# Performance work log

Hardware: AMD Instinct MI355X
Metric: run time of the kernel (lower is better)

The kernel has to match this reference:

```python
import jax, jax.numpy as jnp
import numpy as np

N_NODES = 100000
N_EDGES = 3200000
D_IN = 128
D_OUT = 128


def setup_inputs() -> dict:
    key = jax.random.key(0)
    k1, k2, k3 = jax.random.split(key, 3)
    x = jax.random.normal(k1, (N_NODES, D_IN), dtype=jnp.float32)
    edge_index = jax.random.randint(k2, (2, N_EDGES), 0, N_NODES, dtype=jnp.int64)
    # Glorot-style init for the GCN linear weight [out, in]
    weight = jax.random.normal(k3, (D_OUT, D_IN), dtype=jnp.float32) * (1.0 / np.sqrt(D_IN))
    bias = jnp.zeros((D_OUT,), dtype=jnp.float32)
    return {"x": x, "edge_index": edge_index, "weight": weight, "bias": bias}


def reference(x, edge_index, weight, bias):
    """LinearEncoder.forward: (GCNConv(x, edge_index), 0).

    GCNConv: out = D^-1/2 (A + I) D^-1/2 (x W^T) + b  (symmetric norm, self-loops).
    """
    n = x.shape[0]
    src = edge_index[0]
    dst = edge_index[1]
    # add self-loops
    loops = jnp.arange(n, dtype=src.dtype)
    src = jnp.concatenate([src, loops])
    dst = jnp.concatenate([dst, loops])
    # degree (in-degree over destination nodes, unit edge weights)
    ones = jnp.ones(src.shape[0], dtype=x.dtype)
    deg = jax.ops.segment_sum(ones, dst, num_segments=n)
    deg_inv_sqrt = jnp.where(deg > 0, jax.lax.rsqrt(deg), 0.0).astype(x.dtype)
    norm = deg_inv_sqrt[src] * deg_inv_sqrt[dst]  # [E+N]
    # dense transform first (as in PyG GCNConv), then sparse aggregation
    h = x @ weight.T  # [N, D_OUT]
    msgs = h[src] * norm[:, None]  # [E+N, D_OUT]
    out = jax.ops.segment_sum(msgs, dst, num_segments=n) + bias
    return (out, 0)
```

## Files before the change

### kernel.cpp

```cpp
#include <hip/hip_runtime.h>
#include <hip/hip_bf16.h>

#define N_NODES 100000
#define N_EDGES 3200000
#define D 128

typedef unsigned short u16;

#define BKT_W 512
#define NBKT 196
#define NSH 8
#define CAPS 2304
#define CAPB (NSH * CAPS)
#define EPB 6400
#define P1B 500
#define EPT 25

#define CW_BLOCKS 8

typedef __attribute__((ext_vector_type(8))) short bf16x8;
typedef __attribute__((ext_vector_type(4))) float f32x4;

__device__ __forceinline__ float bf2f(u16 u) {
    union { unsigned i; float f; } a; a.i = ((unsigned)u) << 16; return a.f;
}
__device__ __forceinline__ float asf(unsigned u) {
    union { unsigned i; float f; } a; a.i = u; return a.f;
}
__device__ __forceinline__ u16 f2bf(float f) {
    __hip_bfloat16 b = __float2bfloat16(f);
    return *(u16*)&b;
}

__global__ __launch_bounds__(256) void p1_multisplit(const int* __restrict__ ei,
                                                     int* __restrict__ bcnt,
                                                     unsigned* __restrict__ bbuf) {
    __shared__ unsigned s1[EPB];
    __shared__ unsigned s2[EPB];
    __shared__ int hist[NBKT], lbase[NBKT], cur[NBKT], gbase[NBKT];
    __shared__ int sc[256];
    int t = threadIdx.x, blk = blockIdx.x;
    int sh = blk & (NSH - 1);
    int e0 = blk * EPB;
    if (t < NBKT) hist[t] = 0;
    __syncthreads();

    unsigned char bk[EPT];
#pragma unroll
    for (int k = 0; k < EPT; ++k) {
        int i = k * 256 + t;
        int s = ei[e0 + i];
        int d = ei[N_EDGES + e0 + i];
        unsigned bkt = (unsigned)d >> 9;
        bk[k] = (unsigned char)bkt;
        s1[i] = ((unsigned)s << 9) | ((unsigned)d & 511u);
        atomicAdd(&hist[bkt], 1);
    }
    __syncthreads();

    if (t < NBKT) gbase[t] = atomicAdd(&bcnt[t * NSH + sh], hist[t]);

    sc[t] = (t < NBKT) ? hist[t] : 0;
    __syncthreads();
    for (int o = 1; o < 256; o <<= 1) {
        int u = (t >= o) ? sc[t - o] : 0;
        __syncthreads();
        sc[t] += u;
        __syncthreads();
    }
    if (t < NBKT) { int ex = sc[t] - hist[t]; lbase[t] = ex; cur[t] = ex; }
    __syncthreads();

#pragma unroll
    for (int k = 0; k < EPT; ++k) {
        int i = k * 256 + t;
        int p = atomicAdd(&cur[bk[k]], 1);
        s2[p] = s1[i];
    }
    __syncthreads();

    int wave = t >> 6, lane = t & 63;
    for (int bkt = wave; bkt < NBKT; bkt += 4) {
        int n = hist[bkt], lb = lbase[bkt], gb = gbase[bkt];
        unsigned* dst = bbuf + ((size_t)bkt * NSH + sh) * CAPS;
        for (int j = lane; j < n; j += 64) {
            int p = gb + j;
            if (p < CAPS) dst[p] = s2[lb + j];
        }
    }
}

__global__ __launch_bounds__(256) void p2_localsort(const unsigned* __restrict__ bbuf,
                                                    const int* __restrict__ bcnt,
                                                    int* __restrict__ sorted,
                                                    int* __restrict__ beg_g,
                                                    int* __restrict__ cnt_g,
                                                    float* __restrict__ dinv_g,
                                                    const float* __restrict__ w,
                                                    u16* __restrict__ wbf) {
    __shared__ int hist[BKT_W], cur[BKT_W], shcnt[NSH];
    __shared__ int sc[256];
    int b = blockIdx.x, t = threadIdx.x;

    if (b >= NBKT) {
        int idx = (b - NBKT) * 256 + t;
        const float4* wp = (const float4*)(w + (size_t)idx * 8);
        float4 a = wp[0], bb = wp[1];
        union { u16 h[8]; uint4 v; } o;
        o.h[0] = f2bf(a.x); o.h[1] = f2bf(a.y);
        o.h[2] = f2bf(a.z); o.h[3] = f2bf(a.w);
        o.h[4] = f2bf(bb.x); o.h[5] = f2bf(bb.y);
        o.h[6] = f2bf(bb.z); o.h[7] = f2bf(bb.w);
        ((uint4*)wbf)[idx] = o.v;
        return;
    }

    if (t < NSH) { int m = bcnt[b * NSH + t]; shcnt[t] = m > CAPS ? CAPS : m; }
    hist[t] = 0; hist[t + 256] = 0;
    __syncthreads();

    for (int sh = 0; sh < NSH; ++sh) {
        int m = shcnt[sh];
        const unsigned* p = bbuf + ((size_t)b * NSH + sh) * CAPS;
        for (int i = t; i < m; i += 256) atomicAdd(&hist[p[i] & 511u], 1);
    }
    __syncthreads();

    int a0 = hist[2 * t], a1 = hist[2 * t + 1];
    sc[t] = a0 + a1;
    __syncthreads();
    for (int o = 1; o < 256; o <<= 1) {
        int u = (t >= o) ? sc[t - o] : 0;
        __syncthreads();
        sc[t] += u;
        __syncthreads();
    }
    int exp_ = sc[t] - a0 - a1;
    cur[2 * t] = exp_;
    cur[2 * t + 1] = exp_ + a0;
    __syncthreads();

#pragma unroll
    for (int q = 0; q < 2; ++q) {
        int l = t + q * 256;
        int node = b * BKT_W + l;
        if (node < N_NODES) {
            int c = hist[l];
            cnt_g[node] = c;
            beg_g[node] = b * CAPB + cur[l];
            dinv_g[node] = rsqrtf((float)(c + 1));
        }
    }
    __syncthreads();

    int* dst = sorted + (size_t)b * CAPB;
    for (int sh = 0; sh < NSH; ++sh) {
        int m = shcnt[sh];
        const unsigned* p = bbuf + ((size_t)b * NSH + sh) * CAPS;
        for (int i = t; i < m; i += 256) {
            unsigned ww = p[i];
            int pp = atomicAdd(&cur[ww & 511u], 1);
            dst[pp] = (int)(ww >> 9);
        }
    }
}

__global__ __launch_bounds__(256) void gemm_h(const float* __restrict__ x,
                                              const u16* __restrict__ wbf,
                                              const float* __restrict__ dinv,
                                              u16* __restrict__ h) {
    int t = threadIdx.x;
    int wave = t >> 6, lane = t & 63;
    int n0 = blockIdx.x * 64 + wave * 16;
    int lrow = lane & 15;
    int quad = lane >> 4;

    int arow = n0 + lrow;
    const float* ap = x + (size_t)(arow < N_NODES ? arow : 0) * D;
    bf16x8 afrag[4];
#pragma unroll
    for (int kt = 0; kt < 4; ++kt) {
        int k0 = kt * 32 + quad * 8;
        f32x4 x0 = *(const f32x4*)(ap + k0);
        f32x4 x1 = *(const f32x4*)(ap + k0 + 4);
        bf16x8 a;
        a[0] = (short)f2bf(x0.x); a[1] = (short)f2bf(x0.y);
        a[2] = (short)f2bf(x0.z); a[3] = (short)f2bf(x0.w);
        a[4] = (short)f2bf(x1.x); a[5] = (short)f2bf(x1.y);
        a[6] = (short)f2bf(x1.z); a[7] = (short)f2bf(x1.w);
        afrag[kt] = a;
    }

    float dsc[4];
#pragma unroll
    for (int i = 0; i < 4; ++i) {
        int n = n0 + quad * 4 + i;
        dsc[i] = (n < N_NODES) ? dinv[n] : 0.f;
    }

#pragma unroll
    for (int jt = 0; jt < 8; ++jt) {
        int j0 = jt * 16;
        f32x4 acc = {0.f, 0.f, 0.f, 0.f};
#pragma unroll
        for (int kt = 0; kt < 4; ++kt) {
            int k0 = kt * 32 + quad * 8;
            bf16x8 b = *(const bf16x8*)(wbf + (size_t)(j0 + lrow) * D + k0);
            acc = __builtin_amdgcn_mfma_f32_16x16x32_bf16(afrag[kt], b, acc, 0, 0, 0);
        }
#pragma unroll
        for (int i = 0; i < 4; ++i) {
            int n = n0 + quad * 4 + i;
            if (n < N_NODES) h[(size_t)n * D + j0 + lrow] = f2bf(acc[i] * dsc[i]);
        }
    }
}

__global__ __launch_bounds__(256) void aggregate_h(const u16* __restrict__ h,
                                                   const float* __restrict__ dinv,
                                                   const int* __restrict__ beg_g,
                                                   const int* __restrict__ cnt_g,
                                                   const int* __restrict__ sorted_src,
                                                   const float* __restrict__ bias,
                                                   float* __restrict__ out) {
    int w = threadIdx.x >> 6;
    int l = threadIdx.x & 63;
    int n = blockIdx.x * 4 + w;
    const unsigned* h32 = (const unsigned*)h;

    unsigned us = h32[(size_t)n * 64 + l];
    float acc0 = asf(us << 16);
    float acc1 = asf(us & 0xffff0000u);

    int c = __builtin_amdgcn_readfirstlane(cnt_g[n]);
    int beg = __builtin_amdgcn_readfirstlane(beg_g[n]);
    const int* sp = sorted_src + beg;

    int i = 0;
    for (; i + 16 <= c; i += 16) {
        int s[16];
#pragma unroll
        for (int j = 0; j < 16; ++j) s[j] = sp[i + j];
        unsigned u[16];
#pragma unroll
        for (int j = 0; j < 16; ++j) u[j] = h32[(size_t)s[j] * 64 + l];
#pragma unroll
        for (int j = 0; j < 16; ++j) {
            acc0 += asf(u[j] << 16);
            acc1 += asf(u[j] & 0xffff0000u);
        }
    }
    for (; i + 4 <= c; i += 4) {
        int s0 = sp[i], s1 = sp[i + 1], s2 = sp[i + 2], s3 = sp[i + 3];
        unsigned u0 = h32[(size_t)s0 * 64 + l];
        unsigned u1 = h32[(size_t)s1 * 64 + l];
        unsigned u2 = h32[(size_t)s2 * 64 + l];
        unsigned u3 = h32[(size_t)s3 * 64 + l];
        acc0 += asf(u0 << 16); acc1 += asf(u0 & 0xffff0000u);
        acc0 += asf(u1 << 16); acc1 += asf(u1 & 0xffff0000u);
        acc0 += asf(u2 << 16); acc1 += asf(u2 & 0xffff0000u);
        acc0 += asf(u3 << 16); acc1 += asf(u3 & 0xffff0000u);
    }
    for (; i < c; ++i) {
        unsigned u = h32[(size_t)sp[i] * 64 + l];
        acc0 += asf(u << 16); acc1 += asf(u & 0xffff0000u);
    }

    float dn = dinv[n];
    float2 bs = ((const float2*)bias)[l];
    float2 o;
    o.x = acc0 * dn + bs.x;
    o.y = acc1 * dn + bs.y;
    ((float2*)out)[(size_t)n * 64 + l] = o;

    if (blockIdx.x == 0 && threadIdx.x == 0) out[(size_t)N_NODES * D] = 0.f;
}

extern "C" void kernel_launch(void* const* d_in, const int* in_sizes, int n_in,
                              void* d_out, int out_size, void* d_ws, size_t ws_size,
                              hipStream_t stream) {
    const float* x = (const float*)d_in[0];
    const int* ei = (const int*)d_in[1];
    const float* w = (const float*)d_in[2];
    const float* bias = (const float*)d_in[3];
    float* out = (float*)d_out;

    char* ws = (char*)d_ws;
    size_t o = 0;
    auto alloc = [&](size_t bytes) -> char* {
        char* p = ws + o;
        o = (o + bytes + 511) & ~(size_t)511;
        return p;
    };
    char* regionA = alloc((size_t)N_NODES * D * 2);
    unsigned* bbuf = (unsigned*)regionA;
    u16* h = (u16*)regionA;
    int* sorted = (int*)alloc((size_t)NBKT * CAPB * 4);
    int* cnt = (int*)alloc((size_t)N_NODES * 4);
    int* beg = (int*)alloc((size_t)N_NODES * 4);
    float* dinv = (float*)alloc((size_t)N_NODES * 4);
    int* bcnt = (int*)alloc((size_t)NBKT * NSH * 4);
    u16* wbf = (u16*)alloc((size_t)D * D * 2);

    hipMemsetAsync(bcnt, 0, (size_t)NBKT * NSH * 4, stream);

    p1_multisplit<<<P1B, 256, 0, stream>>>(ei, bcnt, bbuf);
    p2_localsort<<<NBKT + CW_BLOCKS, 256, 0, stream>>>(bbuf, bcnt, sorted, beg, cnt, dinv, w, wbf);
    gemm_h<<<(N_NODES + 63) / 64, 256, 0, stream>>>(x, wbf, dinv, h);
    aggregate_h<<<N_NODES / 4, 256, 0, stream>>>(h, dinv, beg, cnt, sorted, bias, out);
}
```

Measured before the change: 322.1 us.

## Replace two-pass bucket sort with global atomic counting sort, overlap scatter with GEMM

Builds the CSR by destination with a global atomic degree count, a decoupled block-prefix scan using an atomic running total, and an atomic-cursor scatter of source ids. The scatter runs in the same launch as the MFMA GEMM so the two overlap. This drops the multisplit and local-sort staging buffers and their capacity clamps. In exchange it relies on heavy global atomics. Because the scan blocks take their offsets in arbitrary order, each node's edge segment lands at a nondeterministic place, though it stays contiguous.

Result: slower. 645.6 us (+100.4%).

```diff
diff --git a/kernel.cpp b/kernel.cpp
--- a/kernel.cpp
+++ b/kernel.cpp
@@ -7,16 +7,10 @@
 
 typedef unsigned short u16;
 
-#define BKT_W 512
-#define NBKT 196
-#define NSH 8
-#define CAPS 2304
-#define CAPB (NSH * CAPS)
-#define EPB 6400
-#define P1B 500
-#define EPT 25
-
+#define S1B 3125
 #define CW_BLOCKS 8
+#define SCB 3125
+#define GEMM_B 1563
 
 typedef __attribute__((ext_vector_type(8))) short bf16x8;
 typedef __attribute__((ext_vector_type(4))) float f32x4;
@@ -32,78 +26,21 @@
     return *(u16*)&b;
 }
 
-__global__ __launch_bounds__(256) void p1_multisplit(const int* __restrict__ ei,
-                                                     int* __restrict__ bcnt,
-                                                     unsigned* __restrict__ bbuf) {
-    __shared__ unsigned s1[EPB];
-    __shared__ unsigned s2[EPB];
-    __shared__ int hist[NBKT], lbase[NBKT], cur[NBKT], gbase[NBKT];
-    __shared__ int sc[256];
-    int t = threadIdx.x, blk = blockIdx.x;
-    int sh = blk & (NSH - 1);
-    int e0 = blk * EPB;
-    if (t < NBKT) hist[t] = 0;
-    __syncthreads();
-
-    unsigned char bk[EPT];
-#pragma unroll
-    for (int k = 0; k < EPT; ++k) {
-        int i = k * 256 + t;
-        int s = ei[e0 + i];
-        int d = ei[N_EDGES + e0 + i];
-        unsigned bkt = (unsigned)d >> 9;
-        bk[k] = (unsigned char)bkt;
-        s1[i] = ((unsigned)s << 9) | ((unsigned)d & 511u);
-        atomicAdd(&hist[bkt], 1);
-    }
-    __syncthreads();
-
-    if (t < NBKT) gbase[t] = atomicAdd(&bcnt[t * NSH + sh], hist[t]);
-
-    sc[t] = (t < NBKT) ? hist[t] : 0;
-    __syncthreads();
-    for (int o = 1; o < 256; o <<= 1) {
-        int u = (t >= o) ? sc[t - o] : 0;
-        __syncthreads();
-        sc[t] += u;
-        __syncthreads();
-    }
-    if (t < NBKT) { int ex = sc[t] - hist[t]; lbase[t] = ex; cur[t] = ex; }
-    __syncthreads();
-
-#pragma unroll
-    for (int k = 0; k < EPT; ++k) {
-        int i = k * 256 + t;
-        int p = atomicAdd(&cur[bk[k]], 1);
-        s2[p] = s1[i];
-    }
-    __syncthreads();
-
-    int wave = t >> 6, lane = t & 63;
-    for (int bkt = wave; bkt < NBKT; bkt += 4) {
-        int n = hist[bkt], lb = lbase[bkt], gb = gbase[bkt];
-        unsigned* dst = bbuf + ((size_t)bkt * NSH + sh) * CAPS;
-        for (int j = lane; j < n; j += 64) {
-            int p = gb + j;
-            if (p < CAPS) dst[p] = s2[lb + j];
-        }
-    }
-}
-
-__global__ __launch_bounds__(256) void p2_localsort(const unsigned* __restrict__ bbuf,
-                                                    const int* __restrict__ bcnt,
-                                                    int* __restrict__ sorted,
-                                                    int* __restrict__ beg_g,
-                                                    int* __restrict__ cnt_g,
-                                                    float* __restrict__ dinv_g,
-                                                    const float* __restrict__ w,
-                                                    u16* __restrict__ wbf) {
-    __shared__ int hist[BKT_W], cur[BKT_W], shcnt[NSH];
-    __shared__ int sc[256];
-    int b = blockIdx.x, t = threadIdx.x;
-
-    if (b >= NBKT) {
-        int idx = (b - NBKT) * 256 + t;
+__global__ __launch_bounds__(256) void s1_count(const int* __restrict__ ei,
+                                                int* __restrict__ cnt,
+                                                const float* __restrict__ w,
+                                                u16* __restrict__ wbf) {
+    int blk = blockIdx.x, t = threadIdx.x;
+    if (blk < S1B) {
+        int gid = blk * 256 + t;
+        int e = gid * 4;
+        int4 d4 = *(const int4*)(ei + N_EDGES + e);
+        atomicAdd(&cnt[d4.x], 1);
+        atomicAdd(&cnt[d4.y], 1);
+        atomicAdd(&cnt[d4.z], 1);
+        atomicAdd(&cnt[d4.w], 1);
+    } else {
+        int idx = (blk - S1B) * 256 + t;
         const float4* wp = (const float4*)(w + (size_t)idx * 8);
         float4 a = wp[0], bb = wp[1];
         union { u16 h[8]; uint4 v; } o;
@@ -112,107 +49,106 @@
         o.h[4] = f2bf(bb.x); o.h[5] = f2bf(bb.y);
         o.h[6] = f2bf(bb.z); o.h[7] = f2bf(bb.w);
         ((uint4*)wbf)[idx] = o.v;
-        return;
-    }
-
-    if (t < NSH) { int m = bcnt[b * NSH + t]; shcnt[t] = m > CAPS ? CAPS : m; }
-    hist[t] = 0; hist[t + 256] = 0;
+    }
+}
+
+__global__ __launch_bounds__(256) void s2_scan(const int* __restrict__ cnt,
+                                               int* __restrict__ beg,
+                                               int* __restrict__ cur,
+                                               float* __restrict__ dinv,
+                                               int* __restrict__ gtot) {
+    __shared__ int wsum[4], wbase[4];
+    int t = threadIdx.x, lane = t & 63, w = t >> 6;
+    int n = blockIdx.x * 256 + t;
+    int c = (n < N_NODES) ? cnt[n] : 0;
+    int pre = c;
+#pragma unroll
+    for (int o = 1; o < 64; o <<= 1) {
+        int u = __shfl_up(pre, o);
+        if (lane >= o) pre += u;
+    }
+    if (lane == 63) wsum[w] = pre;
     __syncthreads();
-
-    for (int sh = 0; sh < NSH; ++sh) {
-        int m = shcnt[sh];
-        const unsigned* p = bbuf + ((size_t)b * NSH + sh) * CAPS;
-        for (int i = t; i < m; i += 256) atomicAdd(&hist[p[i] & 511u], 1);
+    if (t == 0) {
+        int s0 = wsum[0], s1 = wsum[1], s2 = wsum[2], s3 = wsum[3];
+        int b = atomicAdd(gtot, s0 + s1 + s2 + s3);
+        wbase[0] = b; wbase[1] = b + s0; wbase[2] = b + s0 + s1; wbase[3] = b + s0 + s1 + s2;
     }
     __syncthreads();
-
-    int a0 = hist[2 * t], a1 = hist[2 * t + 1];
-    sc[t] = a0 + a1;
-    __syncthreads();
-    for (int o = 1; o < 256; o <<= 1) {
-        int u = (t >= o) ? sc[t - o] : 0;
-        __syncthreads();
-        sc[t] += u;
-        __syncthreads();
-    }
-    int exp_ = sc[t] - a0 - a1;
-    cur[2 * t] = exp_;
-    cur[2 * t + 1] = exp_ + a0;
-    __syncthreads();
-
-#pragma unroll
-    for (int q = 0; q < 2; ++q) {
-        int l = t + q * 256;
-        int node = b * BKT_W + l;
-        if (node < N_NODES) {
-            int c = hist[l];
-            cnt_g[node] = c;
-            beg_g[node] = b * CAPB + cur[l];
-            dinv_g[node] = rsqrtf((float)(c + 1));
-        }
-    }
-    __syncthreads();
-
-    int* dst = sorted + (size_t)b * CAPB;
-    for (int sh = 0; sh < NSH; ++sh) {
-        int m = shcnt[sh];
-        const unsigned* p = bbuf + ((size_t)b * NSH + sh) * CAPS;
-        for (int i = t; i < m; i += 256) {
-            unsigned ww = p[i];
-            int pp = atomicAdd(&cur[ww & 511u], 1);
-            dst[pp] = (int)(ww >> 9);
-        }
-    }
-}
-
-__global__ __launch_bounds__(256) void gemm_h(const float* __restrict__ x,
-                                              const u16* __restrict__ wbf,
-                                              const float* __restrict__ dinv,
-                                              u16* __restrict__ h) {
-    int t = threadIdx.x;
-    int wave = t >> 6, lane = t & 63;
-    int n0 = blockIdx.x * 64 + wave * 16;
-    int lrow = lane & 15;
-    int quad = lane >> 4;
-
-    int arow = n0 + lrow;
-    const float* ap = x + (size_t)(arow < N_NODES ? arow : 0) * D;
-    bf16x8 afrag[4];
-#pragma unroll
-    for (int kt = 0; kt < 4; ++kt) {
-        int k0 = kt * 32 + quad * 8;
-        f32x4 x0 = *(const f32x4*)(ap + k0);
-        f32x4 x1 = *(const f32x4*)(ap + k0 + 4);
-        bf16x8 a;
-        a[0] = (short)f2bf(x0.x); a[1] = (short)f2bf(x0.y);
-        a[2] = (short)f2bf(x0.z); a[3] = (short)f2bf(x0.w);
-        a[4] = (short)f2bf(x1.x); a[5] = (short)f2bf(x1.y);
-        a[6] = (short)f2bf(x1.z); a[7] = (short)f2bf(x1.w);
-        afrag[kt] = a;
-    }
-
-    float dsc[4];
-#pragma unroll
-    for (int i = 0; i < 4; ++i) {
-        int n = n0 + quad * 4 + i;
-        dsc[i] = (n < N_NODES) ? dinv[n] : 0.f;
-    }
-
-#pragma unroll
-    for (int jt = 0; jt < 8; ++jt) {
-        int j0 = jt * 16;
-        f32x4 acc = {0.f, 0.f, 0.f, 0.f};
+    if (n < N_NODES) {
+        int b = wbase[w] + (pre - c);
+        beg[n] = b;
+        cur[n] = b;
+        dinv[n] = rsqrtf((float)(c + 1));
+    }
+}
+
+__global__ __launch_bounds__(256) void s3_gemm(const int* __restrict__ ei,
+                                               int* __restrict__ cur,
+                                               int* __restrict__ sorted,
+                                               const float* __restrict__ x,
+                                               const u16* __restrict__ wbf,
+                                               const float* __restrict__ dinv,
+                                               u16* __restrict__ h) {
+    int blk = blockIdx.x, t = threadIdx.x;
+    if (blk < GEMM_B) {
+        int wave = t >> 6, lane = t & 63;
+        int n0 = blk * 64 + wave * 16;
+        int lrow = lane & 15;
+        int quad = lane >> 4;
+
+        int arow = n0 + lrow;
+        const float* ap = x + (size_t)(arow < N_NODES ? arow : 0) * D;
+        bf16x8 afrag[4];
 #pragma unroll
         for (int kt = 0; kt < 4; ++kt) {
             int k0 = kt * 32 + quad * 8;
-            bf16x8 b = *(const bf16x8*)(wbf + (size_t)(j0 + lrow) * D + k0);
-            acc = __builtin_amdgcn_mfma_f32_16x16x32_bf16(afrag[kt], b, acc, 0, 0, 0);
-        }
+            f32x4 x0 = *(const f32x4*)(ap + k0);
+            f32x4 x1 = *(const f32x4*)(ap + k0 + 4);
+            bf16x8 a;
+            a[0] = (short)f2bf(x0.x); a[1] = (short)f2bf(x0.y);
+            a[2] = (short)f2bf(x0.z); a[3] = (short)f2bf(x0.w);
+            a[4] = (short)f2bf(x1.x); a[5] = (short)f2bf(x1.y);
+            a[6] = (short)f2bf(x1.z); a[7] = (short)f2bf(x1.w);
+            afrag[kt] = a;
+        }
+
+        float dsc[4];
 #pragma unroll
         for (int i = 0; i < 4; ++i) {
             int n = n0 + quad * 4 + i;
-            if (n < N_NODES) h[(size_t)n * D + j0 + lrow] = f2bf(acc[i] * dsc[i]);
-        }
+            dsc[i] = (n < N_NODES) ? dinv[n] : 0.f;
+        }
+
+#pragma unroll
+        for (int jt = 0; jt < 8; ++jt) {
+            int j0 = jt * 16;
+            f32x4 acc = {0.f, 0.f, 0.f, 0.f};
+#pragma unroll
+            for (int kt = 0; kt < 4; ++kt) {
+                int k0 = kt * 32 + quad * 8;
+                bf16x8 b = *(const bf16x8*)(wbf + (size_t)(j0 + lrow) * D + k0);
+                acc = __builtin_amdgcn_mfma_f32_16x16x32_bf16(afrag[kt], b, acc, 0, 0, 0);
+            }
+#pragma unroll
+            for (int i = 0; i < 4; ++i) {
+                int n = n0 + quad * 4 + i;
+                if (n < N_NODES) h[(size_t)n * D + j0 + lrow] = f2bf(acc[i] * dsc[i]);
+            }
+        }
+    } else {
+        int gid = (blk - GEMM_B) * 256 + t;
+        int e = gid * 4;
+        int4 s4 = *(const int4*)(ei + e);
+        int4 d4 = *(const int4*)(ei + N_EDGES + e);
+        int p0 = atomicAdd(&cur[d4.x], 1);
+        int p1 = atomicAdd(&cur[d4.y], 1);
+        int p2 = atomicAdd(&cur[d4.z], 1);
+        int p3 = atomicAdd(&cur[d4.w], 1);
+        sorted[p0] = s4.x;
+        sorted[p1] = s4.y;
+        sorted[p2] = s4.z;
+        sorted[p3] = s4.w;
     }
 }
 
@@ -292,20 +228,19 @@
         o = (o + bytes + 511) & ~(size_t)511;
         return p;
     };
-    char* regionA = alloc((size_t)N_NODES * D * 2);
-    unsigned* bbuf = (unsigned*)regionA;
-    u16* h = (u16*)regionA;
-    int* sorted = (int*)alloc((size_t)NBKT * CAPB * 4);
-    int* cnt = (int*)alloc((size_t)N_NODES * 4);
+    u16* h = (u16*)alloc((size_t)N_NODES * D * 2);
+    int* sorted = (int*)alloc((size_t)N_EDGES * 4);
+    int* cnt = (int*)alloc((size_t)(N_NODES + 1) * 4);
     int* beg = (int*)alloc((size_t)N_NODES * 4);
+    int* cur = (int*)alloc((size_t)N_NODES * 4);
     float* dinv = (float*)alloc((size_t)N_NODES * 4);
-    int* bcnt = (int*)alloc((size_t)NBKT * NSH * 4);
     u16* wbf = (u16*)alloc((size_t)D * D * 2);
-
-    hipMemsetAsync(bcnt, 0, (size_t)NBKT * NSH * 4, stream);
-
-    p1_multisplit<<<P1B, 256, 0, stream>>>(ei, bcnt, bbuf);
-    p2_localsort<<<NBKT + CW_BLOCKS, 256, 0, stream>>>(bbuf, bcnt, sorted, beg, cnt, dinv, w, wbf);
-    gemm_h<<<(N_NODES + 63) / 64, 256, 0, stream>>>(x, wbf, dinv, h);
+    int* gtot = cnt + N_NODES;
+
+    hipMemsetAsync(cnt, 0, (size_t)(N_NODES + 1) * 4, stream);
+
+    s1_count<<<S1B + CW_BLOCKS, 256, 0, stream>>>(ei, cnt, w, wbf);
+    s2_scan<<<(N_NODES + 255) / 256, 256, 0, stream>>>(cnt, beg, cur, dinv, gtot);
+    s3_gemm<<<GEMM_B + SCB, 256, 0, stream>>>(ei, cur, sorted, x, wbf, dinv, h);
     aggregate_h<<<N_NODES / 4, 256, 0, stream>>>(h, dinv, beg, cnt, sorted, bias, out);
 }
```
